# Optimization experiments

Measured on AMD Instinct MI355X. Metric: run time of the kernel, lower is better.

The kernel has to match this reference:

```python
import jax, jax.numpy as jnp
import numpy as np

B, S, E = 4, 2048, 1024
H, D, F = 16, 64, 4096
EPS = 1e-5


def layer_norm(x, gamma, beta):
    mu = jnp.mean(x, axis=-1, keepdims=True)
    var = jnp.mean(jnp.square(x - mu), axis=-1, keepdims=True)
    return (x - mu) * jax.lax.rsqrt(var + EPS) * gamma + beta


def setup_inputs() -> dict:
    key = jax.random.key(0)
    ks = jax.random.split(key, 8)
    scale = 0.02  # keep logits in a numerically sane range
    X = jax.random.normal(ks[0], (B, S, E), dtype=jnp.float32)
    WQ = jax.random.normal(ks[1], (H, E, D), dtype=jnp.float32) * scale
    WK = jax.random.normal(ks[2], (H, E, D), dtype=jnp.float32) * scale
    WV = jax.random.normal(ks[3], (H, E, D), dtype=jnp.float32) * scale
    WO = jax.random.normal(ks[4], (H * D, E), dtype=jnp.float32) * scale
    gamma = jnp.ones((E,), dtype=jnp.float32)
    beta = jnp.zeros((E,), dtype=jnp.float32)
    W1 = jax.random.normal(ks[5], (E, F), dtype=jnp.float32) * scale
    b1 = jnp.zeros((F,), dtype=jnp.float32)
    W2 = jax.random.normal(ks[6], (F, E), dtype=jnp.float32) * scale
    b2 = jnp.zeros((E,), dtype=jnp.float32)
    return {"X": X, "WQ": WQ, "WK": WK, "WV": WV, "WO": WO,
            "gamma": gamma, "beta": beta, "W1": W1, "b1": b1, "W2": W2, "b2": b2}


def reference(X, WQ, WK, WV, WO, gamma, beta, W1, b1, W2, b2):
    # Batched-over-heads version of the per-head python loop (same math).
    Q = jnp.einsum('bse,hed->bhsd', X, WQ)  # [B,H,S,D]
    K = jnp.einsum('bse,hed->bhsd', X, WK)
    V = jnp.einsum('bse,hed->bhsd', X, WV)
    scores = jnp.einsum('bhsd,bhtd->bhst', Q, K)  # [B,H,S,T]
    # FAITHFUL quirk: torch.softmax(..., dim=1) on a [B,S,S] tensor normalizes
    # over the QUERY axis (axis=2 here), then divides by sqrt(D) AFTER softmax.
    att = jax.nn.softmax(scores, axis=2) / jnp.sqrt(jnp.float32(D))
    vec = jnp.einsum('bhst,bhtd->bhsd', att, V)  # [B,H,S,D]
    att_vec = jnp.transpose(vec, (0, 2, 1, 3)).reshape(X.shape[0], X.shape[1], H * D)
    vector_att = layer_norm(att_vec @ WO + X, gamma, beta)
    vector_ffn = jax.nn.relu(vector_att @ W1 + b1) @ W2 + b2
    return layer_norm(vector_ffn + vector_att, gamma, beta)
```

## Files before the change

kernel.cpp:

```cpp
#include <hip/hip_runtime.h>
#include <cstddef>
#include <cstdint>

#define BB 4
#define SS 2048
#define EE 1024
#define HH 16
#define DD 64
#define FF 4096

typedef unsigned short u16;
typedef __attribute__((ext_vector_type(8))) short short8;
typedef __attribute__((ext_vector_type(4))) short short4v;
typedef __attribute__((ext_vector_type(4))) float f32x4;
typedef __attribute__((ext_vector_type(16))) float f32x16;
typedef __attribute__((ext_vector_type(4))) unsigned u32x4;

__device__ __forceinline__ u16 f2bf(float x) {
    unsigned u = __builtin_bit_cast(unsigned, x);
    u += 0x7fffu + ((u >> 16) & 1u);
    return (u16)(u >> 16);
}
__device__ __forceinline__ float bf2f(u16 h) {
    unsigned u = ((unsigned)h) << 16;
    return __builtin_bit_cast(float, u);
}
__device__ __forceinline__ float ex2(float x) {
    float r;
    asm("v_exp_f32 %0, %1" : "=v"(r) : "v"(x));
    return r;
}
__device__ __forceinline__ unsigned cvtpk(float lo, float hi) {
    unsigned r;
    asm("v_cvt_pk_bf16_f32 %0, %1, %2" : "=v"(r) : "v"(lo), "v"(hi));
    return r;
}
__device__ __forceinline__ void pl32swap(unsigned &a, unsigned &b) {
    asm("s_nop 1\n\tv_permlane32_swap_b32 %0, %1\n\ts_nop 1" : "+v"(a), "+v"(b));
}
__device__ __forceinline__ int sw(int row, int lbyte) {
    return row * 128 + (lbyte ^ ((row & 7) << 4));
}

#define GLD_LDS16(g, l)                                                     \
    __builtin_amdgcn_global_load_lds(                                       \
        (const __attribute__((address_space(1))) void*)(g),                 \
        (__attribute__((address_space(3))) void*)(l), 16, 0, 0)

__global__ __launch_bounds__(256) void cvt_bf(const float* __restrict__ in,
                                              u16* __restrict__ out, int n4) {
    const int i = blockIdx.x * 256 + threadIdx.x;
    if (i < n4) {
        float4 v = reinterpret_cast<const float4*>(in)[i];
        short4v o;
        o.x = (short)f2bf(v.x); o.y = (short)f2bf(v.y);
        o.z = (short)f2bf(v.z); o.w = (short)f2bf(v.w);
        reinterpret_cast<short4v*>(out)[i] = o;
    }
}

__global__ __launch_bounds__(256) void transp_bf(const float* __restrict__ in,
                                                 u16* __restrict__ out, int R, int C) {
    __shared__ float T[64][65];
    const int r0 = blockIdx.x * 64, c0 = blockIdx.y * 64;
    const size_t zoff = (size_t)blockIdx.z * R * C;
    in += zoff; out += zoff;
    const int tid = threadIdx.x;
#pragma unroll 4
    for (int i = 0; i < 16; ++i) {
        int l = tid + i * 256;
        T[l >> 6][l & 63] = in[(size_t)(r0 + (l >> 6)) * C + c0 + (l & 63)];
    }
    __syncthreads();
#pragma unroll 4
    for (int i = 0; i < 16; ++i) {
        int l = tid + i * 256;
        out[(size_t)(c0 + (l >> 6)) * R + r0 + (l & 63)] = f2bf(T[l & 63][l >> 6]);
    }
}

template <int EPI>
__global__ __launch_bounds__(256) void gemm_bf16(const u16* __restrict__ A,
                                                 const u16* __restrict__ BT,
                                                 int K, int N,
                                                 void* __restrict__ Cout,
                                                 const float* __restrict__ bias,
                                                 const void* __restrict__ resid,
                                                 float oscale) {
    __shared__ u16 As[128 * 32];
    __shared__ u16 Bs[128 * 32];
    const int tid = threadIdx.x;
    const int w = tid >> 6, l = tid & 63;
    const int quad = l >> 4, lane16 = l & 15;
    const int wr = (w >> 1) * 64, wc = (w & 1) * 64;
    const int m0 = blockIdx.x * 128, n0 = blockIdx.y * 128;
    const int drow = w * 32 + (l >> 2);
    const int dk = (l & 3) * 8;
    const u16* Ag = A + (size_t)(m0 + drow) * K + dk;
    const u16* Bg = BT + (size_t)(n0 + drow) * K + dk;
    const size_t r16 = (size_t)16 * K;
    u16* AsD = &As[w * 1024];
    u16* BsD = &Bs[w * 1024];

    f32x4 acc[4][4] = {};
    for (int k0 = 0; k0 < K; k0 += 32) {
        __syncthreads();
        GLD_LDS16(Ag + k0, AsD);
        GLD_LDS16(Ag + k0 + r16, AsD + 512);
        GLD_LDS16(Bg + k0, BsD);
        GLD_LDS16(Bg + k0 + r16, BsD + 512);
        __syncthreads();
        short8 af[4], bf[4];
#pragma unroll
        for (int mf = 0; mf < 4; ++mf)
            af[mf] = *(const short8*)&As[(wr + mf * 16 + lane16) * 32 + quad * 8];
#pragma unroll
        for (int nf = 0; nf < 4; ++nf)
            bf[nf] = *(const short8*)&Bs[(wc + nf * 16 + lane16) * 32 + quad * 8];
#pragma unroll
        for (int mf = 0; mf < 4; ++mf)
#pragma unroll
            for (int nf = 0; nf < 4; ++nf)
                acc[mf][nf] = __builtin_amdgcn_mfma_f32_16x16x32_bf16(af[mf], bf[nf], acc[mf][nf], 0, 0, 0);
    }

#pragma unroll
    for (int mf = 0; mf < 4; ++mf) {
        const int row = m0 + wr + mf * 16 + quad * 4;
#pragma unroll
        for (int nf = 0; nf < 4; ++nf) {
            const int col = n0 + wc + nf * 16 + lane16;
#pragma unroll
            for (int r = 0; r < 4; ++r) {
                float v = acc[mf][nf][r];
                const size_t idx = (size_t)(row + r) * N + col;
                if (EPI == 0) {
                    ((u16*)Cout)[idx] = f2bf(v * oscale);
                } else if (EPI == 1) {
                    ((float*)Cout)[idx] = v + ((const float*)resid)[idx];
                } else if (EPI == 2) {
                    v += bias[col];
                    ((u16*)Cout)[idx] = f2bf(fmaxf(v, 0.f));
                } else {
                    v += bias[col] + bf2f(((const u16*)resid)[idx]);
                    ((float*)Cout)[idx] = v;
                }
            }
        }
    }
}

__global__ __launch_bounds__(256) void stats_l(const u16* __restrict__ Qg,
                                               const u16* __restrict__ Kg,
                                               float* __restrict__ Ls) {
    __shared__ u16 Qt[64 * 72];
    const int t0 = blockIdx.x * 128;
    const int bh = blockIdx.y;
    const int b = bh >> 4, h = bh & 15;
    const int tid = threadIdx.x;
    const int w = tid >> 6, l = tid & 63;
    const int quad = l >> 4, lane16 = l & 15;
    const u16* Qp = Qg + (size_t)b * SS * 1024 + h * 64;
    const u16* Kp = Kg + (size_t)b * SS * 1024 + h * 64;
    const int sr = tid >> 3;
    const int dg = (tid & 7) * 8;

    short8 kf[2][2];
#pragma unroll
    for (int nf = 0; nf < 2; ++nf)
#pragma unroll
        for (int ks = 0; ks < 2; ++ks)
            kf[nf][ks] = *(const short8*)(Kp +
                (size_t)(t0 + w * 32 + nf * 16 + lane16) * 1024 + ks * 32 + quad * 8);

    const u16* qsrc0 = Qp + (size_t)sr * 1024 + dg;
    short8 pq0 = *(const short8*)qsrc0;
    short8 pq1 = *(const short8*)(qsrc0 + (size_t)32 * 1024);

    float lcol[2] = {0.f, 0.f};
    for (int st = 0; st < 32; ++st) {
        __syncthreads();
        *(short8*)&Qt[sr * 72 + dg] = pq0;
        *(short8*)&Qt[(sr + 32) * 72 + dg] = pq1;
        __syncthreads();
        if (st + 1 < 32) {
            const u16* qsrc = Qp + (size_t)((st + 1) * 64 + sr) * 1024 + dg;
            pq0 = *(const short8*)qsrc;
            pq1 = *(const short8*)(qsrc + (size_t)32 * 1024);
        }
        f32x4 sc[4][2] = {};
#pragma unroll
        for (int ks = 0; ks < 2; ++ks) {
#pragma unroll
            for (int mf = 0; mf < 4; ++mf) {
                short8 afr = *(const short8*)&Qt[(mf * 16 + lane16) * 72 + ks * 32 + quad * 8];
#pragma unroll
                for (int nf = 0; nf < 2; ++nf)
                    sc[mf][nf] = __builtin_amdgcn_mfma_f32_16x16x32_bf16(afr, kf[nf][ks], sc[mf][nf], 0, 0, 0);
            }
        }
#pragma unroll
        for (int nf = 0; nf < 2; ++nf)
#pragma unroll
            for (int mf = 0; mf < 4; ++mf)
#pragma unroll
                for (int r = 0; r < 4; ++r) lcol[nf] += ex2(sc[mf][nf][r]);
    }
#pragma unroll
    for (int nf = 0; nf < 2; ++nf) {
        lcol[nf] += __shfl_xor(lcol[nf], 32);
        lcol[nf] += __shfl_xor(lcol[nf], 16);
        if (quad == 0)
            Ls[(size_t)bh * SS + t0 + w * 32 + nf * 16 + lane16] = lcol[nf];
    }
}

__global__ __launch_bounds__(256) void vscale(u16* __restrict__ Vtg,
                                              const float* __restrict__ Ls) {
    const int r = blockIdx.x;
    const int b = blockIdx.y;
    const int h = r >> 6;
    const int t0 = threadIdx.x * 8;
    u16* vp = Vtg + (size_t)r * 8192 + b * SS + t0;
    const float* lp = Ls + (size_t)(b * 16 + h) * SS + t0;
    short8 v = *(short8*)vp;
    short8 o;
#pragma unroll
    for (int i = 0; i < 8; ++i)
        o[i] = (short)f2bf(bf2f((u16)v[i]) * (0.125f / lp[i]));
    *(short8*)vp = o;
}

__global__ __launch_bounds__(256) void pv_fused(const u16* __restrict__ Qg,
                                                const u16* __restrict__ Kg,
                                                const u16* __restrict__ Vtg,
                                                u16* __restrict__ vecbf) {
    __shared__ u16 Ks[64 * 64];
    __shared__ u16 Vs[64 * 64];
    const int s0 = blockIdx.x * 128;
    const int bh = blockIdx.y;
    const int b = bh >> 4, h = bh & 15;
    const int tid = threadIdx.x;
    const int w = tid >> 6, l = tid & 63;
    const int l32 = l & 31, hf = l >> 5;
    const u16* Qp = Qg + (size_t)b * SS * 1024 + h * 64;
    const u16* Kp = Kg + (size_t)b * SS * 1024 + h * 64;
    const u16* Vp = Vtg + (size_t)h * 64 * 8192 + (size_t)b * SS;
    const int sr = tid >> 3, dg = (tid & 7) * 8;

    short8 qf[4];
#pragma unroll
    for (int ks = 0; ks < 4; ++ks)
        qf[ks] = *(const short8*)(Qp + (size_t)(s0 + w * 32 + l32) * 1024 + ks * 16 + hf * 8);

    short8 pk0 = *(const short8*)(Kp + (size_t)sr * 1024 + dg);
    short8 pk1 = *(const short8*)(Kp + (size_t)(sr + 32) * 1024 + dg);
    short8 pv0 = *(const short8*)(Vp + (size_t)sr * 8192 + dg);
    short8 pv1 = *(const short8*)(Vp + (size_t)(sr + 32) * 8192 + dg);

    f32x16 acc[2] = {};
    for (int tt = 0; tt < 32; ++tt) {
        __syncthreads();
        *(short8*)((char*)Ks + sw(sr, dg * 2)) = pk0;
        *(short8*)((char*)Ks + sw(sr + 32, dg * 2)) = pk1;
        *(short8*)((char*)Vs + sw(sr, dg * 2)) = pv0;
        *(short8*)((char*)Vs + sw(sr + 32, dg * 2)) = pv1;
        __syncthreads();
        if (tt + 1 < 32) {
            const int t1 = (tt + 1) * 64;
            pk0 = *(const short8*)(Kp + (size_t)(t1 + sr) * 1024 + dg);
            pk1 = *(const short8*)(Kp + (size_t)(t1 + sr + 32) * 1024 + dg);
            pv0 = *(const short8*)(Vp + (size_t)sr * 8192 + t1 + dg);
            pv1 = *(const short8*)(Vp + (size_t)(sr + 32) * 8192 + t1 + dg);
        }
        f32x16 sc0 = {}, sc1 = {};
#pragma unroll
        for (int ks = 0; ks < 4; ++ks) {
            short8 a0 = *(const short8*)((char*)Ks + sw(l32, ks * 32 + hf * 16));
            short8 a1 = *(const short8*)((char*)Ks + sw(32 + l32, ks * 32 + hf * 16));
            sc0 = __builtin_amdgcn_mfma_f32_32x32x16_bf16(a0, qf[ks], sc0, 0, 0, 0);
            sc1 = __builtin_amdgcn_mfma_f32_32x32x16_bf16(a1, qf[ks], sc1, 0, 0, 0);
        }
        unsigned cp0[8], cp1[8];
#pragma unroll
        for (int p = 0; p < 8; ++p) {
            cp0[p] = cvtpk(ex2(sc0[2 * p]), ex2(sc0[2 * p + 1]));
            cp1[p] = cvtpk(ex2(sc1[2 * p]), ex2(sc1[2 * p + 1]));
        }
        short8 pa[4];
#pragma unroll
        for (int ks2 = 0; ks2 < 4; ++ks2) {
            unsigned* cp = (ks2 & 2) ? cp1 : cp0;
            const int c = (ks2 & 1) * 4;
            unsigned w0 = cp[c + 0], w2 = cp[c + 2];
            unsigned w1 = cp[c + 1], w3 = cp[c + 3];
            pl32swap(w0, w2);
            pl32swap(w1, w3);
            u32x4 t4; t4.x = w0; t4.y = w1; t4.z = w2; t4.w = w3;
            pa[ks2] = __builtin_bit_cast(short8, t4);
        }
#pragma unroll
        for (int ks2 = 0; ks2 < 4; ++ks2)
#pragma unroll
            for (int nf = 0; nf < 2; ++nf) {
                short8 bfr = *(const short8*)((char*)Vs + sw(nf * 32 + l32, ks2 * 32 + hf * 16));
                acc[nf] = __builtin_amdgcn_mfma_f32_32x32x16_bf16(pa[ks2], bfr, acc[nf], 0, 0, 0);
            }
    }
#pragma unroll
    for (int nf = 0; nf < 2; ++nf) {
        const int col = h * 64 + nf * 32 + l32;
#pragma unroll
        for (int r = 0; r < 16; ++r) {
            const int srow = s0 + w * 32 + (r & 3) + 8 * (r >> 2) + 4 * hf;
            vecbf[(size_t)(b * SS + srow) * 1024 + col] = f2bf(acc[nf][r]);
        }
    }
}

__global__ __launch_bounds__(256) void ln_bf_kernel(const float* __restrict__ buf,
                                                    const float* __restrict__ g,
                                                    const float* __restrict__ be,
                                                    u16* __restrict__ outbf) {
    const int row = blockIdx.x;
    const int tid = threadIdx.x;
    const float* p = buf + (size_t)row * EE;
    float4 x = reinterpret_cast<const float4*>(p)[tid];
    float s = x.x + x.y + x.z + x.w;
    __shared__ float red[4];
#pragma unroll
    for (int o = 32; o > 0; o >>= 1) s += __shfl_down(s, o);
    const int wid = tid >> 6, lane = tid & 63;
    if (lane == 0) red[wid] = s;
    __syncthreads();
    const float mu = (red[0] + red[1] + red[2] + red[3]) * (1.0f / EE);
    __syncthreads();
    const float dx = x.x - mu, dy = x.y - mu, dz = x.z - mu, dw = x.w - mu;
    float v = dx * dx + dy * dy + dz * dz + dw * dw;
#pragma unroll
    for (int o = 32; o > 0; o >>= 1) v += __shfl_down(v, o);
    if (lane == 0) red[wid] = v;
    __syncthreads();
    const float var = (red[0] + red[1] + red[2] + red[3]) * (1.0f / EE);
    const float rs = rsqrtf(var + 1e-5f);
    float4 gv = reinterpret_cast<const float4*>(g)[tid];
    float4 bv = reinterpret_cast<const float4*>(be)[tid];
    short4v o;
    o.x = (short)f2bf(dx * rs * gv.x + bv.x);
    o.y = (short)f2bf(dy * rs * gv.y + bv.y);
    o.z = (short)f2bf(dz * rs * gv.z + bv.z);
    o.w = (short)f2bf(dw * rs * gv.w + bv.w);
    reinterpret_cast<short4v*>(outbf + (size_t)row * EE)[tid] = o;
}

__global__ __launch_bounds__(256) void ln_kernel(float* __restrict__ buf,
                                                 const float* __restrict__ g,
                                                 const float* __restrict__ be) {
    const int row = blockIdx.x;
    const int tid = threadIdx.x;
    float* p = buf + (size_t)row * EE;
    float4 x = reinterpret_cast<float4*>(p)[tid];
    float s = x.x + x.y + x.z + x.w;
    __shared__ float red[4];
#pragma unroll
    for (int o = 32; o > 0; o >>= 1) s += __shfl_down(s, o);
    const int wid = tid >> 6, lane = tid & 63;
    if (lane == 0) red[wid] = s;
    __syncthreads();
    const float mu = (red[0] + red[1] + red[2] + red[3]) * (1.0f / EE);
    __syncthreads();
    const float dx = x.x - mu, dy = x.y - mu, dz = x.z - mu, dw = x.w - mu;
    float v = dx * dx + dy * dy + dz * dz + dw * dw;
#pragma unroll
    for (int o = 32; o > 0; o >>= 1) v += __shfl_down(v, o);
    if (lane == 0) red[wid] = v;
    __syncthreads();
    const float var = (red[0] + red[1] + red[2] + red[3]) * (1.0f / EE);
    const float rs = rsqrtf(var + 1e-5f);
    float4 gv = reinterpret_cast<const float4*>(g)[tid];
    float4 bv = reinterpret_cast<const float4*>(be)[tid];
    float4 y;
    y.x = dx * rs * gv.x + bv.x;
    y.y = dy * rs * gv.y + bv.y;
    y.z = dz * rs * gv.z + bv.z;
    y.w = dw * rs * gv.w + bv.w;
    reinterpret_cast<float4*>(p)[tid] = y;
}

extern "C" void kernel_launch(void* const* d_in, const int* in_sizes, int n_in,
                              void* d_out, int out_size, void* d_ws, size_t ws_size,
                              hipStream_t stream) {
    const float* X     = (const float*)d_in[0];
    const float* WQ    = (const float*)d_in[1];
    const float* WK    = (const float*)d_in[2];
    const float* WV    = (const float*)d_in[3];
    const float* WO    = (const float*)d_in[4];
    const float* gamma = (const float*)d_in[5];
    const float* beta  = (const float*)d_in[6];
    const float* W1    = (const float*)d_in[7];
    const float* b1    = (const float*)d_in[8];
    const float* W2    = (const float*)d_in[9];
    const float* b2    = (const float*)d_in[10];
    float* out = (float*)d_out;

    char* ws = (char*)d_ws;
    const size_t MB = 1024 * 1024;
    u16* WQT   = (u16*)(ws + 0);
    u16* WKT   = (u16*)(ws + 2 * MB);
    u16* WVT   = (u16*)(ws + 4 * MB);
    u16* WOT   = (u16*)(ws + 6 * MB);
    u16* W1T   = (u16*)(ws + 8 * MB);
    u16* W2T   = (u16*)(ws + 16 * MB);
    float* Ls  = (float*)(ws + 24 * MB);
    u16* Qbf   = (u16*)(ws + 25 * MB);
    u16* Kbf   = (u16*)(ws + 41 * MB);
    u16* Vt    = (u16*)(ws + 57 * MB);
    u16* vecbf = (u16*)(ws + 73 * MB);
    u16* hid   = (u16*)(ws + 25 * MB);
    u16* Xbf   = (u16*)(ws + 89 * MB);
    float* vatt  = (float*)(ws + 105 * MB);
    u16*   ln1bf = (u16*)(ws + 137 * MB);

    const int NT = BB * SS;

    cvt_bf<<<8192, 256, 0, stream>>>(X, Xbf, NT * EE / 4);
    transp_bf<<<dim3(16, 1, 16), 256, 0, stream>>>(WQ, WQT, EE, DD);
    transp_bf<<<dim3(16, 1, 16), 256, 0, stream>>>(WK, WKT, EE, DD);
    transp_bf<<<dim3(16, 1, 16), 256, 0, stream>>>(WV, WVT, EE, DD);
    transp_bf<<<dim3(16, 16, 1), 256, 0, stream>>>(WO, WOT, HH * DD, EE);
    transp_bf<<<dim3(16, 64, 1), 256, 0, stream>>>(W1, W1T, EE, FF);
    transp_bf<<<dim3(64, 16, 1), 256, 0, stream>>>(W2, W2T, FF, EE);

    gemm_bf16<0><<<dim3(64, 8), 256, 0, stream>>>(Xbf, WQT, EE, 1024, Qbf, nullptr, nullptr, 1.44269504089f);
    gemm_bf16<0><<<dim3(64, 8), 256, 0, stream>>>(Xbf, WKT, EE, 1024, Kbf, nullptr, nullptr, 1.0f);
    gemm_bf16<0><<<dim3(8, 64), 256, 0, stream>>>(WVT, Xbf, EE, 8192, Vt, nullptr, nullptr, 1.0f);

    stats_l<<<dim3(SS / 128, BB * HH), 256, 0, stream>>>(Qbf, Kbf, Ls);
    vscale<<<dim3(1024, BB), 256, 0, stream>>>(Vt, Ls);
    pv_fused<<<dim3(SS / 128, BB * HH), 256, 0, stream>>>(Qbf, Kbf, Vt, vecbf);

    gemm_bf16<1><<<dim3(64, 8), 256, 0, stream>>>(vecbf, WOT, EE, 1024, vatt, nullptr, X, 1.0f);
    ln_bf_kernel<<<NT, 256, 0, stream>>>(vatt, gamma, beta, ln1bf);

    gemm_bf16<2><<<dim3(64, 32), 256, 0, stream>>>(ln1bf, W1T, EE, FF, hid, b1, nullptr, 1.0f);
    gemm_bf16<3><<<dim3(64, 8), 256, 0, stream>>>(hid, W2T, FF, 1024, out, b2, ln1bf, 1.0f);

    ln_kernel<<<NT, 256, 0, stream>>>(out, gamma, beta);
}
```

Measured before the change: 630.7 us.

## Replace GEMM with 256x128 double-buffered, swizzled, XCD-remapped MFMA kernel

Replaces the 128x128, 256-thread bf16 GEMM with a 256x128-tile, 512-thread kernel. It uses 32x32x16 MFMAs, a 64-wide K step, XOR-swizzled LDS, and a two-stage async global-to-LDS prefetch gated by vmcnt waits. Workgroup IDs are remapped so consecutive tiles land on the same XCD for L2 reuse, and setprio is raised around the MFMA section. The goal is to hide global load latency and cut per-k-step barrier overhead in all GEMMs. In exchange it needs a larger LDS footprint and adds hand-tuned wait counts that must match the number of loads issued per stage.

```diff
diff --git a/kernel.cpp b/kernel.cpp
--- a/kernel.cpp
+++ b/kernel.cpp
@@ -79,61 +79,95 @@
     }
 }
 
+#define WAITV6 asm volatile("s_waitcnt vmcnt(6)" ::: "memory")
+#define WAITV0 asm volatile("s_waitcnt vmcnt(0)" ::: "memory")
+
+#define STAGE(p, k0u)                                                         \
+    do {                                                                      \
+        _Pragma("unroll")                                                     \
+        for (int i_ = 0; i_ < 4; ++i_)                                        \
+            GLD_LDS16(Ag + (size_t)(i_ * 64) * K + (k0u),                     \
+                      &lds[(p) * 24576 + (i_ * 64 + w * 8) * 64]);            \
+        _Pragma("unroll")                                                     \
+        for (int j_ = 0; j_ < 2; ++j_)                                        \
+            GLD_LDS16(Bg + (size_t)(j_ * 64) * K + (k0u),                     \
+                      &lds[(p) * 24576 + 16384 + (j_ * 64 + w * 8) * 64]);    \
+    } while (0)
+
 template <int EPI>
-__global__ __launch_bounds__(256) void gemm_bf16(const u16* __restrict__ A,
-                                                 const u16* __restrict__ BT,
-                                                 int K, int N,
-                                                 void* __restrict__ Cout,
-                                                 const float* __restrict__ bias,
-                                                 const void* __restrict__ resid,
-                                                 float oscale) {
-    __shared__ u16 As[128 * 32];
-    __shared__ u16 Bs[128 * 32];
+__global__ __launch_bounds__(512, 2) void gemm256(const u16* __restrict__ A,
+                                                  const u16* __restrict__ BT,
+                                                  int K, int N, int gy,
+                                                  void* __restrict__ Cout,
+                                                  const float* __restrict__ bias,
+                                                  const void* __restrict__ resid,
+                                                  float oscale) {
+    __shared__ __align__(16) u16 lds[2 * 24576];
+    const int nwg = gridDim.x;
+    const int bid = blockIdx.x;
+    const int qq = nwg >> 3, rr = nwg & 7;
+    const int xcd = bid & 7, lin = bid >> 3;
+    const int wgid = (xcd < rr ? xcd * (qq + 1) : rr * (qq + 1) + (xcd - rr) * qq) + lin;
+    const int x = wgid / gy, y = wgid % gy;
+    const int m0 = x * 256, n0 = y * 128;
+
     const int tid = threadIdx.x;
     const int w = tid >> 6, l = tid & 63;
-    const int quad = l >> 4, lane16 = l & 15;
-    const int wr = (w >> 1) * 64, wc = (w & 1) * 64;
-    const int m0 = blockIdx.x * 128, n0 = blockIdx.y * 128;
-    const int drow = w * 32 + (l >> 2);
-    const int dk = (l & 3) * 8;
-    const u16* Ag = A + (size_t)(m0 + drow) * K + dk;
-    const u16* Bg = BT + (size_t)(n0 + drow) * K + dk;
-    const size_t r16 = (size_t)16 * K;
-    u16* AsD = &As[w * 1024];
-    u16* BsD = &Bs[w * 1024];
-
-    f32x4 acc[4][4] = {};
-    for (int k0 = 0; k0 < K; k0 += 32) {
-        __syncthreads();
-        GLD_LDS16(Ag + k0, AsD);
-        GLD_LDS16(Ag + k0 + r16, AsD + 512);
-        GLD_LDS16(Bg + k0, BsD);
-        GLD_LDS16(Bg + k0 + r16, BsD + 512);
-        __syncthreads();
-        short8 af[4], bf[4];
-#pragma unroll
-        for (int mf = 0; mf < 4; ++mf)
-            af[mf] = *(const short8*)&As[(wr + mf * 16 + lane16) * 32 + quad * 8];
-#pragma unroll
-        for (int nf = 0; nf < 4; ++nf)
-            bf[nf] = *(const short8*)&Bs[(wc + nf * 16 + lane16) * 32 + quad * 8];
-#pragma unroll
-        for (int mf = 0; mf < 4; ++mf)
-#pragma unroll
-            for (int nf = 0; nf < 4; ++nf)
-                acc[mf][nf] = __builtin_amdgcn_mfma_f32_16x16x32_bf16(af[mf], bf[nf], acc[mf][nf], 0, 0, 0);
-    }
-
-#pragma unroll
-    for (int mf = 0; mf < 4; ++mf) {
-        const int row = m0 + wr + mf * 16 + quad * 4;
-#pragma unroll
-        for (int nf = 0; nf < 4; ++nf) {
-            const int col = n0 + wc + nf * 16 + lane16;
-#pragma unroll
-            for (int r = 0; r < 4; ++r) {
-                float v = acc[mf][nf][r];
-                const size_t idx = (size_t)(row + r) * N + col;
+    const int l32 = l & 31, hf = l >> 5;
+    const int wm = w >> 1, wn = w & 1;
+
+    const int swz = ((l & 7) ^ (l >> 3)) * 8;
+    const u16* Ag = A + (size_t)(m0 + w * 8 + (l >> 3)) * K + swz;
+    const u16* Bg = BT + (size_t)(n0 + w * 8 + (l >> 3)) * K + swz;
+
+    const int NTt = K >> 6;
+    f32x16 acc[2][2] = {};
+
+    STAGE(0, 0);
+    STAGE(1, 64);
+
+    for (int t = 0; t < NTt; ++t) {
+        const int p = t & 1;
+        if (t < NTt - 1) { WAITV6; } else { WAITV0; }
+        __builtin_amdgcn_sched_barrier(0);
+        __builtin_amdgcn_s_barrier();
+        __builtin_amdgcn_sched_barrier(0);
+        __builtin_amdgcn_s_setprio(1);
+        const u16* Ab = &lds[p * 24576];
+        const u16* Bb = &lds[p * 24576 + 16384];
+#pragma unroll
+        for (int kt = 0; kt < 4; ++kt) {
+            const int cs = (((kt * 2 + hf) ^ (l32 & 7)) * 8);
+            short8 af[2], bfr[2];
+#pragma unroll
+            for (int mb = 0; mb < 2; ++mb)
+                af[mb] = *(const short8*)&Ab[(wm * 64 + mb * 32 + l32) * 64 + cs];
+#pragma unroll
+            for (int nb = 0; nb < 2; ++nb)
+                bfr[nb] = *(const short8*)&Bb[(wn * 64 + nb * 32 + l32) * 64 + cs];
+#pragma unroll
+            for (int mb = 0; mb < 2; ++mb)
+#pragma unroll
+                for (int nb = 0; nb < 2; ++nb)
+                    acc[mb][nb] = __builtin_amdgcn_mfma_f32_32x32x16_bf16(af[mb], bfr[nb], acc[mb][nb], 0, 0, 0);
+        }
+        __builtin_amdgcn_s_setprio(0);
+        __builtin_amdgcn_sched_barrier(0);
+        __builtin_amdgcn_s_barrier();
+        __builtin_amdgcn_sched_barrier(0);
+        if (t + 2 < NTt) STAGE(p, (t + 2) * 64);
+    }
+
+#pragma unroll
+    for (int mb = 0; mb < 2; ++mb)
+#pragma unroll
+        for (int nb = 0; nb < 2; ++nb) {
+            const int col = n0 + wn * 64 + nb * 32 + l32;
+#pragma unroll
+            for (int r = 0; r < 16; ++r) {
+                const int row = m0 + wm * 64 + mb * 32 + (r & 3) + 8 * (r >> 2) + 4 * hf;
+                float v = acc[mb][nb][r];
+                const size_t idx = (size_t)row * N + col;
                 if (EPI == 0) {
                     ((u16*)Cout)[idx] = f2bf(v * oscale);
                 } else if (EPI == 1) {
@@ -147,7 +181,6 @@
                 }
             }
         }
-    }
 }
 
 __global__ __launch_bounds__(256) void stats_l(const u16* __restrict__ Qg,
@@ -431,19 +464,19 @@
     transp_bf<<<dim3(16, 64, 1), 256, 0, stream>>>(W1, W1T, EE, FF);
     transp_bf<<<dim3(64, 16, 1), 256, 0, stream>>>(W2, W2T, FF, EE);
 
-    gemm_bf16<0><<<dim3(64, 8), 256, 0, stream>>>(Xbf, WQT, EE, 1024, Qbf, nullptr, nullptr, 1.44269504089f);
-    gemm_bf16<0><<<dim3(64, 8), 256, 0, stream>>>(Xbf, WKT, EE, 1024, Kbf, nullptr, nullptr, 1.0f);
-    gemm_bf16<0><<<dim3(8, 64), 256, 0, stream>>>(WVT, Xbf, EE, 8192, Vt, nullptr, nullptr, 1.0f);
+    gemm256<0><<<256, 512, 0, stream>>>(Xbf, WQT, 1024, 1024, 8, Qbf, nullptr, nullptr, 1.44269504089f);
+    gemm256<0><<<256, 512, 0, stream>>>(Xbf, WKT, 1024, 1024, 8, Kbf, nullptr, nullptr, 1.0f);
+    gemm256<0><<<256, 512, 0, stream>>>(WVT, Xbf, 1024, 8192, 64, Vt, nullptr, nullptr, 1.0f);
 
     stats_l<<<dim3(SS / 128, BB * HH), 256, 0, stream>>>(Qbf, Kbf, Ls);
     vscale<<<dim3(1024, BB), 256, 0, stream>>>(Vt, Ls);
     pv_fused<<<dim3(SS / 128, BB * HH), 256, 0, stream>>>(Qbf, Kbf, Vt, vecbf);
 
-    gemm_bf16<1><<<dim3(64, 8), 256, 0, stream>>>(vecbf, WOT, EE, 1024, vatt, nullptr, X, 1.0f);
+    gemm256<1><<<256, 512, 0, stream>>>(vecbf, WOT, 1024, 1024, 8, vatt, nullptr, X, 1.0f);
     ln_bf_kernel<<<NT, 256, 0, stream>>>(vatt, gamma, beta, ln1bf);
 
-    gemm_bf16<2><<<dim3(64, 32), 256, 0, stream>>>(ln1bf, W1T, EE, FF, hid, b1, nullptr, 1.0f);
-    gemm_bf16<3><<<dim3(64, 8), 256, 0, stream>>>(hid, W2T, FF, 1024, out, b2, ln1bf, 1.0f);
+    gemm256<2><<<1024, 512, 0, stream>>>(ln1bf, W1T, 1024, FF, 32, hid, b1, nullptr, 1.0f);
+    gemm256<3><<<256, 512, 0, stream>>>(hid, W2T, FF, 1024, 8, out, b2, ln1bf, 1.0f);
 
     ln_kernel<<<NT, 256, 0, stream>>>(out, gamma, beta);
 }
```

Result: faster. 586.5 us (-7.0%).
